# Kernel optimization log

Hardware: AMD Instinct MI355X
Metric: run time of the kernel (lower is better)

Reference implementation:

```python
import jax, jax.numpy as jnp
import numpy as np

DT = 1.0
V_TH = 1.0
TAU_MIN = 0.001
R_MIN = 1e-06
BETA = 10.0  # surrogate slope


def setup_inputs() -> dict:
    key = jax.random.key(0)
    k1, k2, k3 = jax.random.split(key, 3)
    T, B, N = 100, 128, 4096
    x = jax.random.normal(k1, (T, B, N), dtype=jnp.float32)
    # learned per-neuron raw params (softplus-parameterized tau and soft-reset)
    # initialized near the module defaults (tau_init=2.0, soft_reset_init=1.0) with noise
    tau_raw0 = float(np.log(np.expm1(2.0 - TAU_MIN)))
    r_raw0 = float(np.log(np.expm1(1.0 - R_MIN)))
    tau_raw = tau_raw0 + 0.1 * jax.random.normal(k2, (N,), dtype=jnp.float32)
    r_raw = r_raw0 + 0.1 * jax.random.normal(k3, (N,), dtype=jnp.float32)
    return {"x": x, "tau_raw": tau_raw, "r_raw": r_raw}


def reference(x, tau_raw, r_raw):
    # x: (T, B, N); tau_raw, r_raw: (N,)
    tau = jax.nn.softplus(tau_raw) + TAU_MIN          # (N,)
    alpha = jnp.exp(-DT / tau)                        # (N,) decay factor
    r = jax.nn.softplus(r_raw) + R_MIN                # (N,) soft-reset amount

    def step(v, xt):
        # v, xt: (B, N)
        v = alpha * v + (1.0 - alpha) * xt
        u = v - V_TH
        hard = (u > 0).astype(xt.dtype)
        soft = jax.nn.sigmoid(BETA * u)
        # forward = hard step; backward = sigmoid derivative (surrogate gradient)
        s = jax.lax.stop_gradient(hard - soft) + soft
        v = v - s * r  # detach_reset=False: gradient flows through reset
        return v, s

    v0 = jnp.zeros(x.shape[1:], dtype=x.dtype)  # (B, N) initial membrane
    _, spikes = jax.lax.scan(step, v0, x)       # spikes: (T, B, N)
    return spikes
```

## Files before the change

### kernel.cpp

```cpp
#include <hip/hip_runtime.h>
#include <cmath>


#define TSTEPS 100

__device__ __forceinline__ float softplus_once(float xr) {
  double x = (double)xr;
  double sp = (x > 0.0) ? (x + log1p(exp(-x))) : log1p(exp(x));
  return (float)sp;
}

__global__ __launch_bounds__(256) void lif_fwd(
    const float* __restrict__ x,
    const float* __restrict__ tau_raw,
    const float* __restrict__ r_raw,
    float* __restrict__ out,
    int B, int N) {
#pragma clang fp contract(off)
  const int nq  = N >> 2;
  const int tid = blockIdx.x * blockDim.x + threadIdx.x;
  if (tid >= B * nq) return;
  const int n0 = (tid % nq) << 2;
  const int b  = tid / nq;

  float4 a4, o4, r4;
  {
    float av[4], ov[4], rv[4];
#pragma unroll
    for (int i = 0; i < 4; ++i) {
      float tau = softplus_once(tau_raw[n0 + i]) + 0.001f;
      float q   = -1.0f / tau;
      float ai  = (float)exp((double)q);
      av[i] = ai;
      ov[i] = 1.0f - ai;
      rv[i] = softplus_once(r_raw[n0 + i]) + 1e-6f;
    }
    a4 = make_float4(av[0], av[1], av[2], av[3]);
    o4 = make_float4(ov[0], ov[1], ov[2], ov[3]);
    r4 = make_float4(rv[0], rv[1], rv[2], rv[3]);
  }

  const size_t base = (size_t)b * (size_t)N + (size_t)n0;
  const size_t str4 = ((size_t)B * (size_t)N) >> 2;
  const float4* xp = (const float4*)x + (base >> 2);
  float4*       op = (float4*)out + (base >> 2);

  float4 v = make_float4(0.f, 0.f, 0.f, 0.f);

  float4 c0 = xp[0];
  float4 c1 = xp[str4];
  const float4* xpre = xp + 2 * str4;

  for (int t = 0; t < TSTEPS; ++t) {
    float4 c2 = make_float4(0.f, 0.f, 0.f, 0.f);
    if (t + 2 < TSTEPS) c2 = *xpre;
    xpre += str4;

    float4 s;
#define LIF_STEP(c)                                                  \
    {                                                                \
      float vn = a4.c * v.c + o4.c * c0.c;  \
      float u  = vn - 1.0f;                                          \
      bool fire = u > 0.0f;                                          \
      s.c = fire ? 1.0f : 0.0f;                                      \
      v.c = fire ? (vn - r4.c) : vn;                                 \
    }
    LIF_STEP(x) LIF_STEP(y) LIF_STEP(z) LIF_STEP(w)
#undef LIF_STEP

    *op = s;
    op += str4;
    c0 = c1;
    c1 = c2;
  }
}

extern "C" void kernel_launch(void* const* d_in, const int* in_sizes, int n_in,
                              void* d_out, int out_size, void* d_ws, size_t ws_size,
                              hipStream_t stream) {
  const float* x       = (const float*)d_in[0];
  const float* tau_raw = (const float*)d_in[1];
  const float* r_raw   = (const float*)d_in[2];
  float*       out     = (float*)d_out;

  const int N = in_sizes[1];
  const int B = in_sizes[0] / (TSTEPS * N);

  const int threads = B * (N >> 2);
  const int block   = 256;
  const int grid    = (threads + block - 1) / block;
  lif_fwd<<<grid, block, 0, stream>>>(x, tau_raw, r_raw, out, B, N);
}
```

Baseline: 352.3 us.

## Use two neurons per thread with deeper prefetch and nontemporal loads/stores

Each thread now handles two neurons using 8-byte vectors instead of four neurons using float4, which doubles the thread count and the parallelism available to hide memory latency. The input prefetch depth grows from 2 to 4 timesteps through an unrolled ring buffer. Loads and stores are marked nontemporal to avoid polluting the cache on this streaming workload. In exchange, each access is narrower, so more memory instructions are issued per byte moved, and each thread recomputes per-neuron parameters for fewer neurons.

```diff
diff --git a/kernel.cpp b/kernel.cpp
--- a/kernel.cpp
+++ b/kernel.cpp
@@ -3,6 +3,9 @@
 
 
 #define TSTEPS 100
+#define PF 4
+
+typedef float f32x2 __attribute__((ext_vector_type(2)));
 
 __device__ __forceinline__ float softplus_once(float xr) {
   double x = (double)xr;
@@ -17,62 +20,73 @@
     float* __restrict__ out,
     int B, int N) {
 #pragma clang fp contract(off)
-  const int nq  = N >> 2;
+  const int nh  = N >> 1;
   const int tid = blockIdx.x * blockDim.x + threadIdx.x;
-  if (tid >= B * nq) return;
-  const int n0 = (tid % nq) << 2;
-  const int b  = tid / nq;
+  if (tid >= B * nh) return;
+  const int n0 = (tid % nh) << 1;
+  const int b  = tid / nh;
 
-  float4 a4, o4, r4;
+  float a0, a1, o0, o1, r0, r1;
   {
-    float av[4], ov[4], rv[4];
-#pragma unroll
-    for (int i = 0; i < 4; ++i) {
-      float tau = softplus_once(tau_raw[n0 + i]) + 0.001f;
-      float q   = -1.0f / tau;
-      float ai  = (float)exp((double)q);
-      av[i] = ai;
-      ov[i] = 1.0f - ai;
-      rv[i] = softplus_once(r_raw[n0 + i]) + 1e-6f;
-    }
-    a4 = make_float4(av[0], av[1], av[2], av[3]);
-    o4 = make_float4(ov[0], ov[1], ov[2], ov[3]);
-    r4 = make_float4(rv[0], rv[1], rv[2], rv[3]);
+    float tau = softplus_once(tau_raw[n0]) + 0.001f;
+    a0 = (float)exp((double)(-1.0f / tau));
+    o0 = 1.0f - a0;
+    r0 = softplus_once(r_raw[n0]) + 1e-6f;
+    tau = softplus_once(tau_raw[n0 + 1]) + 0.001f;
+    a1 = (float)exp((double)(-1.0f / tau));
+    o1 = 1.0f - a1;
+    r1 = softplus_once(r_raw[n0 + 1]) + 1e-6f;
   }
 
-  const size_t base = (size_t)b * (size_t)N + (size_t)n0;
-  const size_t str4 = ((size_t)B * (size_t)N) >> 2;
-  const float4* xp = (const float4*)x + (base >> 2);
-  float4*       op = (float4*)out + (base >> 2);
+  const size_t base2 = ((size_t)b * (size_t)N + (size_t)n0) >> 1;
+  const size_t str2  = ((size_t)B * (size_t)N) >> 1;
+  const f32x2* xp = (const f32x2*)x + base2;
+  f32x2*       op = (f32x2*)out + base2;
 
-  float4 v = make_float4(0.f, 0.f, 0.f, 0.f);
+  float v0 = 0.f, v1 = 0.f;
 
-  float4 c0 = xp[0];
-  float4 c1 = xp[str4];
-  const float4* xpre = xp + 2 * str4;
+  f32x2 buf[PF];
+#pragma unroll
+  for (int j = 0; j < PF; ++j)
+    buf[j] = __builtin_nontemporal_load(&xp[(size_t)j * str2]);
+  const f32x2* xl = xp + (size_t)PF * str2;
 
-  for (int t = 0; t < TSTEPS; ++t) {
-    float4 c2 = make_float4(0.f, 0.f, 0.f, 0.f);
-    if (t + 2 < TSTEPS) c2 = *xpre;
-    xpre += str4;
+#define LIF_STEP(c)                                               \
+  {                                                               \
+    f32x2 s;                                                      \
+    {                                                             \
+      float vn = a0 * v0 + o0 * (c)[0];  \
+      float u  = vn - 1.0f;                                       \
+      bool fire = u > 0.0f;                                       \
+      s[0] = fire ? 1.0f : 0.0f;                                  \
+      v0   = fire ? (vn - r0) : vn;                               \
+    }                                                             \
+    {                                                             \
+      float vn = a1 * v1 + o1 * (c)[1];                           \
+      float u  = vn - 1.0f;                                       \
+      bool fire = u > 0.0f;                                       \
+      s[1] = fire ? 1.0f : 0.0f;                                  \
+      v1   = fire ? (vn - r1) : vn;                               \
+    }                                                             \
+    __builtin_nontemporal_store(s, op);                           \
+    op += str2;                                                   \
+  }
 
-    float4 s;
-#define LIF_STEP(c)                                                  \
-    {                                                                \
-      float vn = a4.c * v.c + o4.c * c0.c;  \
-      float u  = vn - 1.0f;                                          \
-      bool fire = u > 0.0f;                                          \
-      s.c = fire ? 1.0f : 0.0f;                                      \
-      v.c = fire ? (vn - r4.c) : vn;                                 \
+  for (int t = 0; t < TSTEPS - PF; t += PF) {
+#pragma unroll
+    for (int j = 0; j < PF; ++j) {
+      f32x2 c = buf[j];
+      buf[j] = __builtin_nontemporal_load(xl);
+      xl += str2;
+      LIF_STEP(c)
     }
-    LIF_STEP(x) LIF_STEP(y) LIF_STEP(z) LIF_STEP(w)
+  }
+#pragma unroll
+  for (int j = 0; j < PF; ++j) {
+    f32x2 c = buf[j];
+    LIF_STEP(c)
+  }
 #undef LIF_STEP
-
-    *op = s;
-    op += str4;
-    c0 = c1;
-    c1 = c2;
-  }
 }
 
 extern "C" void kernel_launch(void* const* d_in, const int* in_sizes, int n_in,
@@ -86,7 +100,8 @@
   const int N = in_sizes[1];
   const int B = in_sizes[0] / (TSTEPS * N);
 
-  const int threads = B * (N >> 2);
+  const int threads = B * (N >> 1);
+  if (threads <= 0) return;
   const int block   = 256;
   const int grid    = (threads + block - 1) / block;
   lif_fwd<<<grid, block, 0, stream>>>(x, tau_raw, r_raw, out, B, N);
```

After: 338.6 us (median of 2 runs). 1.04x faster.
